# Performance work log

Hardware: AMD Instinct MI355X
Metric: run time of the kernel (lower is better)

The kernel has to match this reference:

```python
import jax, jax.numpy as jnp
import numpy as np

ID_LENGTH = 4   # number of identity images cached in the id bank
HEADS = 20      # SDXL attention heads at channel 1280
SA32 = 0.5


def setup_inputs() -> dict:
    key = jax.random.key(0)
    ks = jax.random.split(key, 7)
    B2, T, C = 8, 576, 1280            # 2*id_length images, 576 tokens each (768/32)^2
    S = ID_LENGTH * T                   # 2304 grouped sequence length
    hidden_states = jax.random.normal(ks[0], (B2, T, C), jnp.float32)
    # cal_attn_mask_xl: one random row pattern repeated, with each image's own
    # block forced True (sliced to the [:id_length*T, :id_length*T] write-mode mask)
    row_pat = jax.random.uniform(ks[1], (1, S)) < SA32
    mask = jnp.tile(row_pat, (S, 1))
    img = jnp.arange(S) // T
    mask = mask | (img[:, None] == img[None, :])
    w = lambda k: jax.random.normal(k, (C, C), jnp.float32) * 0.02
    return {
        "hidden_states": hidden_states,
        "mask": mask,
        "Wq": w(ks[2]), "Wk": w(ks[3]), "Wv": w(ks[4]), "Wo": w(ks[5]),
        "bo": jnp.zeros((C,), jnp.float32),
    }


def reference(hidden_states, mask, Wq, Wk, Wv, Wo, bo):
    # __call1__ path: regroup [2*id_length, T, C] -> [2, id_length*T, C]
    B2, T, C = hidden_states.shape
    hs = hidden_states.reshape(2, ID_LENGTH * T, C)
    hd = C // HEADS

    def split_heads(x):  # [2, S, C] -> [2, H, S, hd]
        return x.reshape(2, -1, HEADS, hd).transpose(0, 2, 1, 3)

    q = split_heads(hs @ Wq)
    k = split_heads(hs @ Wk)   # write mode: encoder_hidden_states == hidden_states
    v = split_heads(hs @ Wv)

    scores = jnp.einsum('bhqd,bhkd->bhqk', q, k) / jnp.sqrt(jnp.asarray(hd, q.dtype))
    scores = jnp.where(mask[None, None], scores, jnp.finfo(scores.dtype).min)
    attnw = jax.nn.softmax(scores, axis=-1)
    out = jnp.einsum('bhqk,bhkd->bhqd', attnw, v)
    out = out.transpose(0, 2, 1, 3).reshape(2, -1, C)
    out = out @ Wo + bo                 # attn.to_out[0]
    return out.reshape(B2, T, C)
```

## Files before the change

### kernel.cpp

```cpp
#include <hip/hip_runtime.h>
#include <hip/hip_bf16.h>
#include <stdint.h>
#include <math.h>

#define S_TOT 2304
#define C_DIM 1280
#define NHEAD 20
#define HD    64
#define M_TOT 4608
#define BH_STRIDE (S_TOT * HD)
#define SC_ROWS 2624
#define KC_STRIDE (SC_ROWS * 64)
#define LOG2E 1.44269504088896f
#define C_SC  (0.125f * LOG2E)
#define MFIX  12.0f
#define QBLK  192

typedef __attribute__((ext_vector_type(8))) short bf16x8;
typedef __attribute__((ext_vector_type(4))) float f32x4;

__device__ __forceinline__ short f2bf(float f) {
    union { float f; uint32_t u; } v; v.f = f;
    uint32_t r = v.u + 0x7FFFu + ((v.u >> 16) & 1u);
    return (short)(r >> 16);
}

__device__ __forceinline__ uint32_t pack2bf(float a, float b) {
    __hip_bfloat162 h = __float22bfloat162_rn(make_float2(a, b));
    union { __hip_bfloat162 h; uint32_t u; } cv; cv.h = h; return cv.u;
}

__device__ __forceinline__ f32x4 zero4() {
    f32x4 z; z[0] = 0.f; z[1] = 0.f; z[2] = 0.f; z[3] = 0.f; return z;
}

__device__ __forceinline__ void gload_lds16(const void* g, void* l) {
    __builtin_amdgcn_global_load_lds(
        (const __attribute__((address_space(1))) uint32_t*)g,
        (__attribute__((address_space(3))) uint32_t*)l, 16, 0, 0);
}

__global__ __launch_bounds__(256)
void prologue(const float* __restrict__ hs, short* __restrict__ hsb,
              const float* __restrict__ W0, const float* __restrict__ W1,
              const float* __restrict__ W2, const float* __restrict__ W3,
              short* __restrict__ T0, short* __restrict__ T1,
              short* __restrict__ T2, short* __restrict__ T3,
              const int* __restrict__ mask, int* __restrict__ hdr,
              int* __restrict__ destmap) {
    __shared__ float tile[32][33];
    __shared__ unsigned long long wbits[36];
    __shared__ int pp[36], dd[36], hb[9];

    const int bx = blockIdx.x;
    const int t = threadIdx.x;

    if (bx < 2880) {
        const int i = bx * 256 + t;
        const float4 v0 = reinterpret_cast<const float4*>(hs)[i * 2];
        const float4 v1 = reinterpret_cast<const float4*>(hs)[i * 2 + 1];
        bf16x8 o;
        o[0] = f2bf(v0.x); o[1] = f2bf(v0.y); o[2] = f2bf(v0.z); o[3] = f2bf(v0.w);
        o[4] = f2bf(v1.x); o[5] = f2bf(v1.y); o[6] = f2bf(v1.z); o[7] = f2bf(v1.w);
        reinterpret_cast<bf16x8*>(hsb)[i] = o;
    } else if (bx < 9280) {
        int id = bx - 2880;
        const int z = id / 1600; id -= z * 1600;
        const int by = id / 40, bxx = id - by * 40;
        const float* W; short* T;
        switch (z) {
            case 0:  W = W0; T = T0; break;
            case 1:  W = W1; T = T1; break;
            case 2:  W = W2; T = T2; break;
            default: W = W3; T = T3; break;
        }
        const int tx = t & 31, ty = t >> 5;
        const int k0 = by * 32, n0 = bxx * 32;
#pragma unroll
        for (int i = 0; i < 4; ++i)
            tile[ty + i * 8][tx] = W[(size_t)(k0 + ty + i * 8) * C_DIM + n0 + tx];
        __syncthreads();
#pragma unroll
        for (int i = 0; i < 4; ++i)
            T[(size_t)(n0 + ty + i * 8) * C_DIM + k0 + tx] = f2bf(tile[tx][ty + i * 8]);
    } else {
        for (int it = 0; it < 9; ++it) {
            const int k = it * 256 + t;
            const int src = (k < 1152) ? 1152 : 0;
            const bool pat = mask[(size_t)src * S_TOT + k] != 0;
            unsigned long long b = __ballot(pat);
            if ((t & 63) == 0) wbits[it * 4 + (t >> 6)] = b;
        }
        __syncthreads();
        if (t == 0) {
            int pcum = 0, dcum[4] = {0, 0, 0, 0};
            for (int wdx = 0; wdx < 36; ++wdx) {
                const int img = wdx / 9;
                const int pc = __popcll(wbits[wdx]);
                pp[wdx] = pcum; dd[wdx] = dcum[img];
                pcum += pc; dcum[img] += 64 - pc;
            }
            hb[0] = pcum;
            int base = (pcum + 63) & ~63;
            for (int i = 0; i < 4; ++i) {
                hb[1 + i] = base; hb[5 + i] = dcum[i];
                base += (dcum[i] + 63) & ~63;
            }
            for (int i = 0; i < 9; ++i) hdr[i] = hb[i];
        }
        __syncthreads();
        if (t < 36) {
            const unsigned long long w64 = wbits[t];
            const int img = t / 9;
            const int pbase = pp[t], dbase = hb[1 + img] + dd[t];
            int pc = 0, dc = 0;
            for (int b = 0; b < 64; ++b) {
                if ((w64 >> b) & 1) destmap[t * 64 + b] = pbase + (pc++);
                else                destmap[t * 64 + b] = dbase + (dc++);
            }
        }
    }
}

__global__ __launch_bounds__(256)
void zero_pads(const int* __restrict__ hdr, short* __restrict__ Kc,
               short* __restrict__ Vr) {
    const int bh = blockIdx.x;
    const int t = threadIdx.x;
    short* Kb = Kc + (size_t)bh * KC_STRIDE;
    short* Vb = Vr + (size_t)bh * KC_STRIDE;
    for (int seg = 0; seg < 5; ++seg) {
        const int cnt = (seg == 0) ? hdr[0] : hdr[4 + seg];
        const int sb  = (seg == 0) ? 0      : hdr[seg];
        const int s0 = sb + cnt;
        const int nrows = ((cnt + 63) & ~63) - cnt;
        for (int idx = t; idx < nrows * 64; idx += 256) {
            const int r = idx >> 6, d = idx & 63;
            Kb[(size_t)(s0 + r) * 64 + d] = 0;
            Vb[(size_t)(s0 + r) * 64 + d] = 0;
        }
    }
}

__global__ __launch_bounds__(256)
void transp_v(const short* __restrict__ Vr, short* __restrict__ Vc) {
    __shared__ short tile[64][72];
    const int bh = blockIdx.y;
    const int s0 = blockIdx.x * 64;
    const int t = threadIdx.x;
    const short* src = Vr + (size_t)bh * KC_STRIDE;
    short* dst = Vc + (size_t)bh * KC_STRIDE;

#pragma unroll
    for (int i = 0; i < 2; ++i) {
        const int e = (i * 256 + t) * 8;
        const int r = e >> 6, c = e & 63;
        bf16x8 v = *(const bf16x8*)(src + (size_t)(s0 + r) * 64 + c);
        *(bf16x8*)&tile[r][c] = v;
    }
    __syncthreads();
    const int d = t & 63, c0 = (t >> 6) * 16;
    short tmp[16];
#pragma unroll
    for (int j = 0; j < 16; ++j) tmp[j] = tile[c0 + j][d];
    *(bf16x8*)(dst + (size_t)d * SC_ROWS + s0 + c0) = *(const bf16x8*)tmp;
    *(bf16x8*)(dst + (size_t)d * SC_ROWS + s0 + c0 + 8) = *(const bf16x8*)(tmp + 8);
}

__global__ __launch_bounds__(256)
void gemm_qkv3(const short* __restrict__ hsb,
               const short* __restrict__ Wtq, const short* __restrict__ Wtk,
               const short* __restrict__ Wtv, const int* __restrict__ destmap,
               short* __restrict__ Qb, short* __restrict__ Kc, short* __restrict__ Vr) {
    __shared__ short As[2][128 * 64];
    __shared__ short Bs[2][3][128 * 64];
    __shared__ int dm[128];

    const int bid = blockIdx.x;
    const int vid = (bid & 7) * 45 + (bid >> 3);
    const int n0 = (vid / 36) * 128, m0 = (vid % 36) * 128;
    const int t = threadIdx.x;
    const int lane = t & 63, w = t >> 6;
    const int g = lane >> 4, l15 = lane & 15;
    const int wm = w >> 1, wn = w & 1;

    if (t < 128) {
        const int s0 = (m0 >= S_TOT) ? m0 - S_TOT : m0;
        dm[t] = destmap[s0 + t];
    }

    f32x4 acc[3][4][4];
#pragma unroll
    for (int z = 0; z < 3; ++z)
#pragma unroll
        for (int mi = 0; mi < 4; ++mi)
#pragma unroll
            for (int ni = 0; ni < 4; ++ni) acc[z][mi][ni] = zero4();

    auto stage = [&](int k0, int buf) {
#pragma unroll
        for (int i = 0; i < 4; ++i) {
            const int F = i * 4096 + t * 16;
            const int row = F >> 7;
            const int colb = (F & 127) ^ ((row & 7) << 4);
            gload_lds16((const char*)hsb + ((size_t)(m0 + row) * C_DIM + k0) * 2 + colb,
                        (char*)As[buf] + F);
        }
#pragma unroll
        for (int z = 0; z < 3; ++z) {
            const short* Wt = (z == 0) ? Wtq : (z == 1) ? Wtk : Wtv;
#pragma unroll
            for (int i = 0; i < 4; ++i) {
                const int F = i * 4096 + t * 16;
                const int row = F >> 7;
                const int colb = (F & 127) ^ ((row & 7) << 4);
                gload_lds16((const char*)Wt + ((size_t)(n0 + row) * C_DIM + k0) * 2 + colb,
                            (char*)Bs[buf][z] + F);
            }
        }
    };

    stage(0, 0);
    asm volatile("s_waitcnt vmcnt(0)" ::: "memory");
    __builtin_amdgcn_s_barrier();
    __builtin_amdgcn_sched_barrier(0);

    const int nsteps = C_DIM / 64;
    for (int s = 0; s < nsteps; ++s) {
        const int cur = s & 1;
        if (s + 1 < nsteps) stage((s + 1) * 64, cur ^ 1);

        const char* Ac = (const char*)As[cur];
#pragma unroll
        for (int ks = 0; ks < 2; ++ks) {
            const int kb = ks * 64 + g * 16;
            bf16x8 af[4];
#pragma unroll
            for (int mi = 0; mi < 4; ++mi) {
                const int row = wm * 64 + mi * 16 + l15;
                af[mi] = *(const bf16x8*)(Ac + row * 128 + (kb ^ ((row & 7) << 4)));
            }
#pragma unroll
            for (int z = 0; z < 3; ++z) {
                const char* Bc = (const char*)Bs[cur][z];
                bf16x8 bfr[4];
#pragma unroll
                for (int ni = 0; ni < 4; ++ni) {
                    const int row = wn * 64 + ni * 16 + l15;
                    bfr[ni] = *(const bf16x8*)(Bc + row * 128 + (kb ^ ((row & 7) << 4)));
                }
                __builtin_amdgcn_s_setprio(1);
#pragma unroll
                for (int mi = 0; mi < 4; ++mi)
#pragma unroll
                    for (int ni = 0; ni < 4; ++ni)
                        acc[z][mi][ni] = __builtin_amdgcn_mfma_f32_16x16x32_bf16(
                            af[mi], bfr[ni], acc[z][mi][ni], 0, 0, 0);
                __builtin_amdgcn_s_setprio(0);
            }
        }

        asm volatile("s_waitcnt vmcnt(0)" ::: "memory");
        __builtin_amdgcn_s_barrier();
        __builtin_amdgcn_sched_barrier(0);
    }

#pragma unroll
    for (int z = 0; z < 3; ++z)
#pragma unroll
        for (int mi = 0; mi < 4; ++mi)
#pragma unroll
            for (int ni = 0; ni < 4; ++ni)
#pragma unroll
                for (int r = 0; r < 4; ++r) {
                    const int m = m0 + wm * 64 + mi * 16 + g * 4 + r;
                    const int n = n0 + wn * 64 + ni * 16 + l15;
                    const int bg = (m >= S_TOT) ? 1 : 0;
                    const int s = m - bg * S_TOT;
                    const int h = n >> 6, d = n & 63;
                    const size_t bh = (size_t)(bg * NHEAD + h);
                    float aval = acc[z][mi][ni][r];
                    if (z == 0) aval *= C_SC;
                    const short v = f2bf(aval);
                    if (z == 0) {
                        Qb[bh * BH_STRIDE + (size_t)s * HD + d] = v;
                    } else {
                        const int sc = dm[m - m0];
                        short* dst = (z == 1) ? Kc : Vr;
                        dst[bh * (size_t)KC_STRIDE + (size_t)sc * 64 + d] = v;
                    }
                }
}

__device__ __forceinline__ void gemm_core(const short* __restrict__ A,
                                          const short* __restrict__ Wt,
                                          int m0, int n0,
                                          f32x4 acc[4][4],
                                          short* AsB, short* BsB) {
    const int t = threadIdx.x;
    const int lane = t & 63, w = t >> 6;
    const int g = lane >> 4, l15 = lane & 15;
    const int wm = w >> 1, wn = w & 1;

#pragma unroll
    for (int mi = 0; mi < 4; ++mi)
#pragma unroll
        for (int ni = 0; ni < 4; ++ni) acc[mi][ni] = zero4();

    auto stage = [&](int k0, int buf) {
#pragma unroll
        for (int i = 0; i < 4; ++i) {
            const int F = i * 4096 + t * 16;
            const int row = F >> 7;
            const int b = F & 127;
            const int colb = b ^ ((row & 7) << 4);
            gload_lds16((const char*)A + ((size_t)(m0 + row) * C_DIM + k0) * 2 + colb,
                        (char*)AsB + buf * 16384 + F);
            gload_lds16((const char*)Wt + ((size_t)(n0 + row) * C_DIM + k0) * 2 + colb,
                        (char*)BsB + buf * 16384 + F);
        }
    };

    stage(0, 0);
    asm volatile("s_waitcnt vmcnt(0)" ::: "memory");
    __builtin_amdgcn_s_barrier();
    __builtin_amdgcn_sched_barrier(0);

    int cur = 0;
    for (int k0 = 0; k0 < C_DIM; k0 += 64) {
        if (k0 + 64 < C_DIM) stage(k0 + 64, cur ^ 1);
        const char* Ac = (const char*)AsB + cur * 16384;
        const char* Bc = (const char*)BsB + cur * 16384;
#pragma unroll
        for (int ks = 0; ks < 2; ++ks) {
            const int kb = ks * 64 + g * 16;
            bf16x8 af[4], bfr[4];
#pragma unroll
            for (int mi = 0; mi < 4; ++mi) {
                const int row = wm * 64 + mi * 16 + l15;
                af[mi] = *(const bf16x8*)(Ac + row * 128 + (kb ^ ((row & 7) << 4)));
            }
#pragma unroll
            for (int ni = 0; ni < 4; ++ni) {
                const int row = wn * 64 + ni * 16 + l15;
                bfr[ni] = *(const bf16x8*)(Bc + row * 128 + (kb ^ ((row & 7) << 4)));
            }
            __builtin_amdgcn_s_setprio(1);
#pragma unroll
            for (int mi = 0; mi < 4; ++mi)
#pragma unroll
                for (int ni = 0; ni < 4; ++ni)
                    acc[mi][ni] = __builtin_amdgcn_mfma_f32_16x16x32_bf16(
                        af[mi], bfr[ni], acc[mi][ni], 0, 0, 0);
            __builtin_amdgcn_s_setprio(0);
        }
        asm volatile("s_waitcnt vmcnt(0)" ::: "memory");
        __builtin_amdgcn_s_barrier();
        __builtin_amdgcn_sched_barrier(0);
        cur ^= 1;
    }
}

__global__ __launch_bounds__(256)
void gemm_out(const short* __restrict__ Ab, const short* __restrict__ Wto,
              const float* __restrict__ bo, float* __restrict__ out) {
    __shared__ short As[2 * 128 * 64];
    __shared__ short Bs[2 * 128 * 64];
    const int bid = blockIdx.x;
    const int vid = (bid & 7) * 45 + (bid >> 3);
    const int n0 = (vid / 36) * 128, m0 = (vid % 36) * 128;

    f32x4 acc[4][4];
    gemm_core(Ab, Wto, m0, n0, acc, As, Bs);

    const int t = threadIdx.x;
    const int lane = t & 63, w = t >> 6, g = lane >> 4, l15 = lane & 15;
    const int wm = w >> 1, wn = w & 1;
#pragma unroll
    for (int mi = 0; mi < 4; ++mi)
#pragma unroll
        for (int ni = 0; ni < 4; ++ni) {
            const int n = n0 + wn * 64 + ni * 16 + l15;
            const float bias = bo[n];
#pragma unroll
            for (int r = 0; r < 4; ++r) {
                const int m = m0 + wm * 64 + mi * 16 + g * 4 + r;
                out[(size_t)m * C_DIM + n] = acc[mi][ni][r] + bias;
            }
        }
}

__global__ __launch_bounds__(768)
void attn_mfma(const short* __restrict__ Qb, const short* __restrict__ Kc,
               const short* __restrict__ Vc, const int* __restrict__ hdr,
               short* __restrict__ Ab) {
    __shared__ short Ks[3][4096];
    __shared__ short Vs[3][4096];
    __shared__ short Ps[QBLK * 64];

    const int t = threadIdx.x;
    const int lane = t & 63, w = t >> 6, g = lane >> 4, l15 = lane & 15;
    const int bid = blockIdx.x;
    const int vid = (bid & 7) * 60 + (bid >> 3);
    const int bh_i = vid / 12, qb = vid % 12;
    const int b = bh_i / NHEAD, h = bh_i % NHEAD;
    const int q0 = qb * QBLK;
    const size_t bh = (size_t)bh_i;
    const int qimg = qb / 3;

    const int cntp  = hdr[0];
    const int dbase = hdr[1 + qimg];
    const int cntd  = hdr[5 + qimg];
    const int ntp = (cntp + 63) >> 6, ntd = (cntd + 63) >> 6, nt = ntp + ntd;

    const short* Qp = Qb + bh * BH_STRIDE;
    const short* Kp = Kc + bh * (size_t)KC_STRIDE;
    const short* Vp = Vc + bh * (size_t)KC_STRIDE;

    bf16x8 qf[2];
    {
        const int row = q0 + w * 16 + l15;
        qf[0] = *(const bf16x8*)(Qp + (size_t)row * HD + g * 8);
        qf[1] = *(const bf16x8*)(Qp + (size_t)row * HD + 32 + g * 8);
    }

    bf16x8 onesv;
#pragma unroll
    for (int j = 0; j < 8; ++j) onesv[j] = (short)0x3F80;

    const f32x4 sinit = {-MFIX, -MFIX, -MFIX, -MFIX};
    f32x4 o_acc[4], lacc;
#pragma unroll
    for (int df = 0; df < 4; ++df) o_acc[df] = zero4();
    lacc = zero4();

    const int rowP = w * 16 + l15;
    const int swzP = (rowP & 7) << 4;
    const int ckbase = g * 4;

    auto tstart = [&](int tt) {
        return (tt < ntp) ? tt * 64 : dbase + (tt - ntp) * 64;
    };
    auto stage = [&](int start, int bufsel) {
        if (t < 512) {
            const int F = t * 16;
            const int row = F >> 7, bb = F & 127;
            const int colb = bb ^ ((row & 7) << 4);
            gload_lds16((const char*)Kp + (size_t)(start + row) * 128 + colb,
                        (char*)Ks[bufsel] + F);
            gload_lds16((const char*)Vp + (size_t)row * (SC_ROWS * 2) + start * 2 + colb,
                        (char*)Vs[bufsel] + F);
        }
    };

    stage(tstart(0), 0);
    if (nt > 1) stage(tstart(1), 1);
    asm volatile("s_waitcnt vmcnt(2)" ::: "memory");
    __builtin_amdgcn_s_barrier();
    __builtin_amdgcn_sched_barrier(0);

    for (int tt = 0; tt < nt; ++tt) {
        const int cur = tt % 3;
        if (tt + 2 < nt) stage(tstart(tt + 2), (tt + 2) % 3);
        const int lim = (tt < ntp) ? cntp - tt * 64 : cntd - (tt - ntp) * 64;

        f32x4 sacc[4];
#pragma unroll
        for (int nf = 0; nf < 4; ++nf) sacc[nf] = sinit;
        __builtin_amdgcn_s_setprio(1);
#pragma unroll
        for (int ks = 0; ks < 2; ++ks) {
            const int kb = ks * 64 + g * 16;
#pragma unroll
            for (int nf = 0; nf < 4; ++nf) {
                const int row = nf * 16 + l15;
                bf16x8 kf = *(const bf16x8*)((const char*)Ks[cur] + row * 128 + (kb ^ ((row & 7) << 4)));
                sacc[nf] = __builtin_amdgcn_mfma_f32_16x16x32_bf16(kf, qf[ks], sacc[nf], 0, 0, 0);
            }
        }
        __builtin_amdgcn_s_setprio(0);

        if (lim < 64) {
#pragma unroll
            for (int nf = 0; nf < 4; ++nf)
#pragma unroll
                for (int r = 0; r < 4; ++r)
                    if (nf * 16 + ckbase + r >= lim) sacc[nf][r] = -1e30f;
        }

#pragma unroll
        for (int nf = 0; nf < 4; ++nf) {
            uint2 u;
            u.x = pack2bf(__builtin_amdgcn_exp2f(sacc[nf][0]),
                          __builtin_amdgcn_exp2f(sacc[nf][1]));
            u.y = pack2bf(__builtin_amdgcn_exp2f(sacc[nf][2]),
                          __builtin_amdgcn_exp2f(sacc[nf][3]));
            *(uint2*)((char*)Ps + rowP * 128 + ((nf * 32 + g * 8) ^ swzP)) = u;
        }

        __builtin_amdgcn_s_setprio(1);
#pragma unroll
        for (int ks = 0; ks < 2; ++ks) {
            const int kb = ks * 64 + g * 16;
            bf16x8 pf = *(const bf16x8*)((const char*)Ps + rowP * 128 + (kb ^ swzP));
            lacc = __builtin_amdgcn_mfma_f32_16x16x32_bf16(onesv, pf, lacc, 0, 0, 0);
#pragma unroll
            for (int df = 0; df < 4; ++df) {
                const int rowV = df * 16 + l15;
                bf16x8 vf = *(const bf16x8*)((const char*)Vs[cur] + rowV * 128 + (kb ^ ((rowV & 7) << 4)));
                o_acc[df] = __builtin_amdgcn_mfma_f32_16x16x32_bf16(vf, pf, o_acc[df], 0, 0, 0);
            }
        }
        __builtin_amdgcn_s_setprio(0);

        asm volatile("s_waitcnt vmcnt(2)" ::: "memory");
        __builtin_amdgcn_s_barrier();
        __builtin_amdgcn_sched_barrier(0);
    }

    const float inv = 1.f / lacc[0];
    const int rowg = b * S_TOT + q0 + w * 16 + l15;
#pragma unroll
    for (int df = 0; df < 4; ++df) {
        uint2 u;
        u.x = pack2bf(o_acc[df][0] * inv, o_acc[df][1] * inv);
        u.y = pack2bf(o_acc[df][2] * inv, o_acc[df][3] * inv);
        *(uint2*)(Ab + (size_t)rowg * C_DIM + h * 64 + df * 16 + g * 4) = u;
    }
}

extern "C" void kernel_launch(void* const* d_in, const int* in_sizes, int n_in,
                              void* d_out, int out_size, void* d_ws, size_t ws_size,
                              hipStream_t stream)
{
    const float* hs   = (const float*)d_in[0];
    const int*   mask = (const int*)  d_in[1];
    const float* Wq   = (const float*)d_in[2];
    const float* Wk   = (const float*)d_in[3];
    const float* Wv   = (const float*)d_in[4];
    const float* Wo   = (const float*)d_in[5];
    const float* bo   = (const float*)d_in[6];
    float* out = (float*)d_out;

    char* ws = (char*)d_ws;
    const size_t mat_b = (size_t)M_TOT * C_DIM * 2;
    const size_t w_b   = (size_t)C_DIM * C_DIM * 2;
    const size_t kc_b  = (size_t)40 * KC_STRIDE * 2;

    short* hsb = (short*)ws;                 ws += mat_b;
    short* Wtq = (short*)ws;                 ws += w_b;
    short* Wtk = (short*)ws;                 ws += w_b;
    short* Wtv = (short*)ws;                 ws += w_b;
    short* Wto = (short*)ws;                 ws += w_b;
    short* Qb  = (short*)ws;                 ws += mat_b;
    short* Kc  = (short*)ws;                 ws += kc_b;
    short* Vr  = (short*)ws;                 ws += kc_b;
    short* Vc  = (short*)ws;                 ws += kc_b;
    short* Ab  = (short*)ws;                 ws += mat_b;
    int*   hdr = (int*)ws;                   ws += 64;
    int*   destmap = (int*)ws;               ws += S_TOT * 4;

    prologue<<<9281, 256, 0, stream>>>(hs, hsb, Wq, Wk, Wv, Wo,
                                       Wtq, Wtk, Wtv, Wto, mask, hdr, destmap);
    zero_pads<<<40, 256, 0, stream>>>(hdr, Kc, Vr);

    gemm_qkv3<<<360, 256, 0, stream>>>(
        hsb, Wtq, Wtk, Wtv, destmap, Qb, Kc, Vr);

    transp_v<<<dim3(SC_ROWS / 64, 40), 256, 0, stream>>>(Vr, Vc);

    attn_mfma<<<480, 768, 0, stream>>>(Qb, Kc, Vc, hdr, Ab);

    gemm_out<<<360, 256, 0, stream>>>(Ab, Wto, bo, out);
}
```

Measured before the change: 195.4 us.

## Split fused QKV GEMM across 12 waves, one output matrix per wave group

The fused QKV projection kernel now launches 768 threads per block. Each group of four waves computes only one of Q, K or V, sharing the staged A tile, so each thread holds 16 accumulators instead of 48. This is meant to cut register pressure and raise the number of waves available to hide MFMA and LDS latency, at the cost of more A-fragment LDS reads across groups. Separately, the attention loop now drains all outstanding loads (vmcnt 0) on iterations that issue no prefetch, which fixes the wait count near the end of the loop.

```diff
diff --git a/kernel.cpp b/kernel.cpp
--- a/kernel.cpp
+++ b/kernel.cpp
@@ -167,13 +167,13 @@
     *(bf16x8*)(dst + (size_t)d * SC_ROWS + s0 + c0 + 8) = *(const bf16x8*)(tmp + 8);
 }
 
-__global__ __launch_bounds__(256)
+__global__ __launch_bounds__(768, 3)
 void gemm_qkv3(const short* __restrict__ hsb,
                const short* __restrict__ Wtq, const short* __restrict__ Wtk,
                const short* __restrict__ Wtv, const int* __restrict__ destmap,
                short* __restrict__ Qb, short* __restrict__ Kc, short* __restrict__ Vr) {
-    __shared__ short As[2][128 * 64];
-    __shared__ short Bs[2][3][128 * 64];
+    __shared__ short As[2 * 8192];
+    __shared__ short Bs[6 * 8192];
     __shared__ int dm[128];
 
     const int bid = blockIdx.x;
@@ -182,40 +182,39 @@
     const int t = threadIdx.x;
     const int lane = t & 63, w = t >> 6;
     const int g = lane >> 4, l15 = lane & 15;
-    const int wm = w >> 1, wn = w & 1;
+    const int z = w >> 2;
+    const int wm = (w >> 1) & 1, wn = w & 1;
 
     if (t < 128) {
         const int s0 = (m0 >= S_TOT) ? m0 - S_TOT : m0;
         dm[t] = destmap[s0 + t];
     }
 
-    f32x4 acc[3][4][4];
-#pragma unroll
-    for (int z = 0; z < 3; ++z)
-#pragma unroll
-        for (int mi = 0; mi < 4; ++mi)
-#pragma unroll
-            for (int ni = 0; ni < 4; ++ni) acc[z][mi][ni] = zero4();
+    f32x4 acc[4][4];
+#pragma unroll
+    for (int mi = 0; mi < 4; ++mi)
+#pragma unroll
+        for (int ni = 0; ni < 4; ++ni) acc[mi][ni] = zero4();
 
     auto stage = [&](int k0, int buf) {
+        const int tt = t & 255, zg = t >> 8;
+        const short* Wt = (zg == 0) ? Wtq : (zg == 1) ? Wtk : Wtv;
 #pragma unroll
         for (int i = 0; i < 4; ++i) {
-            const int F = i * 4096 + t * 16;
+            const int F = i * 4096 + tt * 16;
             const int row = F >> 7;
             const int colb = (F & 127) ^ ((row & 7) << 4);
-            gload_lds16((const char*)hsb + ((size_t)(m0 + row) * C_DIM + k0) * 2 + colb,
-                        (char*)As[buf] + F);
-        }
-#pragma unroll
-        for (int z = 0; z < 3; ++z) {
-            const short* Wt = (z == 0) ? Wtq : (z == 1) ? Wtk : Wtv;
+            gload_lds16((const char*)Wt + ((size_t)(n0 + row) * C_DIM + k0) * 2 + colb,
+                        (char*)Bs + (buf * 3 + zg) * 16384 + F);
+        }
+        if (zg == 0) {
 #pragma unroll
             for (int i = 0; i < 4; ++i) {
-                const int F = i * 4096 + t * 16;
+                const int F = i * 4096 + tt * 16;
                 const int row = F >> 7;
                 const int colb = (F & 127) ^ ((row & 7) << 4);
-                gload_lds16((const char*)Wt + ((size_t)(n0 + row) * C_DIM + k0) * 2 + colb,
-                            (char*)Bs[buf][z] + F);
+                gload_lds16((const char*)hsb + ((size_t)(m0 + row) * C_DIM + k0) * 2 + colb,
+                            (char*)As + buf * 16384 + F);
             }
         }
     };
@@ -230,34 +229,30 @@
         const int cur = s & 1;
         if (s + 1 < nsteps) stage((s + 1) * 64, cur ^ 1);
 
-        const char* Ac = (const char*)As[cur];
+        const char* Ac = (const char*)As + cur * 16384;
+        const char* Bc = (const char*)Bs + (cur * 3 + z) * 16384;
 #pragma unroll
         for (int ks = 0; ks < 2; ++ks) {
             const int kb = ks * 64 + g * 16;
-            bf16x8 af[4];
+            bf16x8 af[4], bfr[4];
 #pragma unroll
             for (int mi = 0; mi < 4; ++mi) {
                 const int row = wm * 64 + mi * 16 + l15;
                 af[mi] = *(const bf16x8*)(Ac + row * 128 + (kb ^ ((row & 7) << 4)));
             }
 #pragma unroll
-            for (int z = 0; z < 3; ++z) {
-                const char* Bc = (const char*)Bs[cur][z];
-                bf16x8 bfr[4];
-#pragma unroll
-                for (int ni = 0; ni < 4; ++ni) {
-                    const int row = wn * 64 + ni * 16 + l15;
-                    bfr[ni] = *(const bf16x8*)(Bc + row * 128 + (kb ^ ((row & 7) << 4)));
-                }
-                __builtin_amdgcn_s_setprio(1);
-#pragma unroll
-                for (int mi = 0; mi < 4; ++mi)
-#pragma unroll
-                    for (int ni = 0; ni < 4; ++ni)
-                        acc[z][mi][ni] = __builtin_amdgcn_mfma_f32_16x16x32_bf16(
-                            af[mi], bfr[ni], acc[z][mi][ni], 0, 0, 0);
-                __builtin_amdgcn_s_setprio(0);
-            }
+            for (int ni = 0; ni < 4; ++ni) {
+                const int row = wn * 64 + ni * 16 + l15;
+                bfr[ni] = *(const bf16x8*)(Bc + row * 128 + (kb ^ ((row & 7) << 4)));
+            }
+            __builtin_amdgcn_s_setprio(1);
+#pragma unroll
+            for (int mi = 0; mi < 4; ++mi)
+#pragma unroll
+                for (int ni = 0; ni < 4; ++ni)
+                    acc[mi][ni] = __builtin_amdgcn_mfma_f32_16x16x32_bf16(
+                        af[mi], bfr[ni], acc[mi][ni], 0, 0, 0);
+            __builtin_amdgcn_s_setprio(0);
         }
 
         asm volatile("s_waitcnt vmcnt(0)" ::: "memory");
@@ -266,30 +261,26 @@
     }
 
 #pragma unroll
-    for (int z = 0; z < 3; ++z)
-#pragma unroll
-        for (int mi = 0; mi < 4; ++mi)
-#pragma unroll
-            for (int ni = 0; ni < 4; ++ni)
-#pragma unroll
-                for (int r = 0; r < 4; ++r) {
-                    const int m = m0 + wm * 64 + mi * 16 + g * 4 + r;
-                    const int n = n0 + wn * 64 + ni * 16 + l15;
-                    const int bg = (m >= S_TOT) ? 1 : 0;
-                    const int s = m - bg * S_TOT;
-                    const int h = n >> 6, d = n & 63;
-                    const size_t bh = (size_t)(bg * NHEAD + h);
-                    float aval = acc[z][mi][ni][r];
-                    if (z == 0) aval *= C_SC;
-                    const short v = f2bf(aval);
-                    if (z == 0) {
-                        Qb[bh * BH_STRIDE + (size_t)s * HD + d] = v;
-                    } else {
-                        const int sc = dm[m - m0];
-                        short* dst = (z == 1) ? Kc : Vr;
-                        dst[bh * (size_t)KC_STRIDE + (size_t)sc * 64 + d] = v;
-                    }
+    for (int mi = 0; mi < 4; ++mi)
+#pragma unroll
+        for (int ni = 0; ni < 4; ++ni)
+#pragma unroll
+            for (int r = 0; r < 4; ++r) {
+                const int m = m0 + wm * 64 + mi * 16 + g * 4 + r;
+                const int n = n0 + wn * 64 + ni * 16 + l15;
+                const int bg = (m >= S_TOT) ? 1 : 0;
+                const int s = m - bg * S_TOT;
+                const int h = n >> 6, d = n & 63;
+                const size_t bh = (size_t)(bg * NHEAD + h);
+                const float aval = acc[mi][ni][r];
+                if (z == 0) {
+                    Qb[bh * BH_STRIDE + (size_t)s * HD + d] = f2bf(aval * C_SC);
+                } else {
+                    const int sc = dm[m - m0];
+                    short* dst = (z == 1) ? Kc : Vr;
+                    dst[bh * (size_t)KC_STRIDE + (size_t)sc * 64 + d] = f2bf(aval);
                 }
+            }
 }
 
 __device__ __forceinline__ void gemm_core(const short* __restrict__ A,
@@ -461,7 +452,8 @@
 
     for (int tt = 0; tt < nt; ++tt) {
         const int cur = tt % 3;
-        if (tt + 2 < nt) stage(tstart(tt + 2), (tt + 2) % 3);
+        const bool pre = (tt + 2 < nt);
+        if (pre) stage(tstart(tt + 2), (tt + 2) % 3);
         const int lim = (tt < ntp) ? cntp - tt * 64 : cntd - (tt - ntp) * 64;
 
         f32x4 sacc[4];
@@ -513,7 +505,8 @@
         }
         __builtin_amdgcn_s_setprio(0);
 
-        asm volatile("s_waitcnt vmcnt(2)" ::: "memory");
+        if (pre) { asm volatile("s_waitcnt vmcnt(2)" ::: "memory"); }
+        else     { asm volatile("s_waitcnt vmcnt(0)" ::: "memory"); }
         __builtin_amdgcn_s_barrier();
         __builtin_amdgcn_sched_barrier(0);
     }
@@ -564,7 +557,7 @@
                                        Wtq, Wtk, Wtv, Wto, mask, hdr, destmap);
     zero_pads<<<40, 256, 0, stream>>>(hdr, Kc, Vr);
 
-    gemm_qkv3<<<360, 256, 0, stream>>>(
+    gemm_qkv3<<<360, 768, 0, stream>>>(
         hsb, Wtq, Wtk, Wtv, destmap, Qb, Kc, Vr);
 
     transp_v<<<dim3(SC_ROWS / 64, 40), 256, 0, stream>>>(Vr, Vc);
```

Result: slower. 210.3 us (+7.7%).
